# Kernel optimization log

Measured on AMD Instinct MI355X. Metric: run time of the kernel, lower is better.

Reference implementation:

```python
import jax, jax.numpy as jnp
import numpy as np

N_NODES = 100000


def _gcn_conv(x, src, dst, deg_inv_sqrt, W, b, num_nodes):
    # GCNConv: out = D^{-1/2} (A+I) D^{-1/2} (x W) + b, with self-loops already
    # appended to (src, dst) and deg_inv_sqrt precomputed over the augmented graph.
    h = x @ W                                            # [N, out]
    coef = deg_inv_sqrt[src] * deg_inv_sqrt[dst]         # [E+N]
    msg = h[src] * coef[:, None]                         # gather + normalize
    out = jax.ops.segment_sum(msg, dst, num_segments=num_nodes)  # scatter-add
    return out + b


def setup_inputs() -> dict:
    key = jax.random.key(0)
    ks = jax.random.split(key, 8)
    n, d, h = N_NODES, 16, 16
    E = 3_200_000
    x = jax.random.normal(ks[0], (n, d), dtype=jnp.float32)
    edge_index = jax.random.randint(ks[1], (2, E), 0, n, dtype=jnp.int64)
    # Glorot-ish init for weights, zeros for biases (as in GCNConv/Linear defaults)
    W1 = jax.random.normal(ks[2], (d, h), dtype=jnp.float32) / np.sqrt(d)
    b1 = jnp.zeros((h,), dtype=jnp.float32)
    W2 = jax.random.normal(ks[3], (h, h), dtype=jnp.float32) / np.sqrt(h)
    b2 = jnp.zeros((h,), dtype=jnp.float32)
    Wfc = jax.random.normal(ks[4], (h, 1), dtype=jnp.float32) / np.sqrt(h)
    bfc = jnp.zeros((1,), dtype=jnp.float32)
    return {"x": x, "edge_index": edge_index, "W1": W1, "b1": b1,
            "W2": W2, "b2": b2, "Wfc": Wfc, "bfc": bfc}


def reference(x, edge_index, W1, b1, W2, b2, Wfc, bfc):
    n = x.shape[0]
    loops = jnp.arange(n, dtype=edge_index.dtype)
    src = jnp.concatenate([edge_index[0], loops])
    dst = jnp.concatenate([edge_index[1], loops])
    # symmetric normalization over graph with self-loops (edge weight 1)
    deg = jax.ops.segment_sum(jnp.ones_like(dst, dtype=x.dtype), dst, num_segments=n)
    deg_inv_sqrt = jnp.where(deg > 0, jax.lax.rsqrt(deg), 0.0)
    h = jax.nn.relu(_gcn_conv(x, src, dst, deg_inv_sqrt, W1, b1, n))
    h = jax.nn.relu(_gcn_conv(h, src, dst, deg_inv_sqrt, W2, b2, n))
    return h @ Wfc + bfc  # [N, 1]
```

## Files before the change

### kernel.cpp

```cpp
#include <hip/hip_runtime.h>
#include <hip/hip_fp16.h>
#include <stdint.h>


constexpr int F = 16;
constexpr int K_MAX = 256;
constexpr int BN = 400;
constexpr int PT = 4096;
constexpr int NPB = 32;
constexpr unsigned int CAP = 14848;

__device__ __forceinline__ float2 h2f2(__half2 h) { return __half22float2(h); }
__device__ __forceinline__ unsigned int bkt400(unsigned int d) {
    return (unsigned int)(((unsigned long long)d * 167773ull) >> 26);
}

__global__ void __launch_bounds__(256)
partition_kernel(const int* __restrict__ src, const int* __restrict__ dst,
                 unsigned int* __restrict__ gcur, unsigned int* __restrict__ recs,
                 int E, int K) {
    __shared__ unsigned int hist[K_MAX * 4];
    __shared__ unsigned int offs[K_MAX * 4];
    __shared__ unsigned int gb[K_MAX];
    __shared__ unsigned int wsum[4];
    __shared__ unsigned int drec[PT];
    __shared__ unsigned char dbuk[PT];
    const int t = threadIdx.x;
    const int tile0 = blockIdx.x * PT;
    const int cnt = min(PT, E - tile0);
    const unsigned int myc = (unsigned int)(t & 3);
    for (int i = t; i < K * 4; i += 256) hist[i] = 0u;
    __syncthreads();
    unsigned int rec[16], bp[16];
#pragma unroll
    for (int k = 0; k < 4; ++k) {
        const int i = t * 4 + k * 1024;
        const int e = tile0 + i;
        if (i + 3 < cnt) {
            int4 s4 = *(const int4*)&src[e];
            int4 d4 = *(const int4*)&dst[e];
            int ss[4] = {s4.x, s4.y, s4.z, s4.w};
            int dd[4] = {d4.x, d4.y, d4.z, d4.w};
#pragma unroll
            for (int u = 0; u < 4; ++u) {
                unsigned int d = (unsigned int)dd[u];
                unsigned int s = (unsigned int)ss[u];
                unsigned int b = bkt400(d);
                rec[k * 4 + u] = ((d - b * (unsigned int)BN) << 17) | s;
                unsigned int pos = atomicAdd(&hist[b * 4 + myc], 1u);
                bp[k * 4 + u] = (b << 14) | (myc << 12) | pos;
            }
        } else {
#pragma unroll
            for (int u = 0; u < 4; ++u) {
                const int ii = i + u;
                bp[k * 4 + u] = 0xFFFFFFFFu;
                if (ii < cnt) {
                    unsigned int d = (unsigned int)dst[tile0 + ii];
                    unsigned int s = (unsigned int)src[tile0 + ii];
                    unsigned int b = bkt400(d);
                    rec[k * 4 + u] = ((d - b * (unsigned int)BN) << 17) | s;
                    unsigned int pos = atomicAdd(&hist[b * 4 + myc], 1u);
                    bp[k * 4 + u] = (b << 14) | (myc << 12) | pos;
                }
            }
        }
    }
    __syncthreads();
    const int lane = t & 63, wid = t >> 6;
    unsigned int tot = 0u;
    if (t < K) {
        unsigned int h0 = hist[t * 4 + 0], h1 = hist[t * 4 + 1];
        unsigned int h2 = hist[t * 4 + 2], h3 = hist[t * 4 + 3];
        tot = h0 + h1 + h2 + h3;
        offs[t * 4 + 0] = 0u;
        offs[t * 4 + 1] = h0;
        offs[t * 4 + 2] = h0 + h1;
        offs[t * 4 + 3] = h0 + h1 + h2;
    }
    unsigned int incl = tot;
#pragma unroll
    for (int o = 1; o < 64; o <<= 1) {
        unsigned int y = __shfl_up(incl, o, 64);
        if (lane >= o) incl += y;
    }
    if (lane == 63) wsum[wid] = incl;
    __syncthreads();
    if (t == 0) {
        unsigned int run = 0;
#pragma unroll
        for (int i = 0; i < 4; ++i) { unsigned int tmp = wsum[i]; wsum[i] = run; run += tmp; }
    }
    __syncthreads();
    if (t < K) {
        unsigned int bb = wsum[wid] + incl - tot;
        unsigned int g = (unsigned int)t * CAP + atomicAdd(&gcur[t], tot);
        gb[t] = g - bb;
        offs[t * 4 + 0] += bb;
        offs[t * 4 + 1] += bb;
        offs[t * 4 + 2] += bb;
        offs[t * 4 + 3] += bb;
    }
    __syncthreads();
#pragma unroll
    for (int k = 0; k < 16; ++k) {
        if (bp[k] != 0xFFFFFFFFu) {
            unsigned int b = bp[k] >> 14, c = (bp[k] >> 12) & 3u, pos = bp[k] & 0xFFFu;
            unsigned int idx = offs[b * 4 + c] + pos;
            drec[idx] = rec[k];
            dbuk[idx] = (unsigned char)b;
        }
    }
    __syncthreads();
    for (int i = t; i < cnt; i += 256) {
        unsigned int b = dbuk[i];
        recs[gb[b] + (unsigned int)i] = drec[i];
    }
}

__global__ void __launch_bounds__(1024)
sort_mv_kernel(const unsigned int* __restrict__ recs, const unsigned int* __restrict__ gcur,
               const float* __restrict__ x, const float* __restrict__ W1,
               float* __restrict__ dis, unsigned int* __restrict__ rp,
               unsigned int* __restrict__ recs2, __half* __restrict__ hs1, int N) {
    __shared__ unsigned int cnt0[BN];
    __shared__ unsigned int cnt1[BN];
    __shared__ unsigned int wsum[7];
    __shared__ float sdis[BN];
    __shared__ float ws[16][16];
    __shared__ float xs[64][17];
    __shared__ unsigned int srt[CAP];
    const int b = blockIdx.x;
    const int t = threadIdx.x;
    const int lane = t & 63, wid = t >> 6;
    if (t < BN) { cnt0[t] = 0u; cnt1[t] = 0u; }
    if (t < 256) ws[t >> 4][t & 15] = W1[t];
    __syncthreads();
    const unsigned int e0 = (unsigned int)b * CAP;
    const unsigned int len = gcur[b];
    const unsigned int len4 = len & ~3u;
    unsigned int* mycnt = (t & 1) ? cnt1 : cnt0;
    for (unsigned int i = 4u * t; i < len4; i += 4096u) {
        uint4 r4 = *(const uint4*)&recs[e0 + i];
        atomicAdd(&mycnt[r4.x >> 17], 1u);
        atomicAdd(&mycnt[r4.y >> 17], 1u);
        atomicAdd(&mycnt[r4.z >> 17], 1u);
        atomicAdd(&mycnt[r4.w >> 17], 1u);
    }
    for (unsigned int i = len4 + t; i < len; i += 1024u)
        atomicAdd(&mycnt[recs[e0 + i] >> 17], 1u);
    __syncthreads();
    unsigned int c = 0, c0v = 0, xsc = 0;
    if (t < BN) {
        c0v = cnt0[t];
        c = c0v + cnt1[t];
        xsc = c;
#pragma unroll
        for (int o = 1; o < 64; o <<= 1) {
            unsigned int y = __shfl_up(xsc, o, 64);
            if (lane >= o) xsc += y;
        }
        if (lane == 63 || t == BN - 1) wsum[wid] = xsc;
    }
    __syncthreads();
    if (t == 0) {
        unsigned int run = 0;
#pragma unroll
        for (int i = 0; i < 7; ++i) { unsigned int tmp = wsum[i]; wsum[i] = run; run += tmp; }
    }
    __syncthreads();
    if (t < BN) {
        const unsigned int srel = wsum[wid] + xsc - c;
        const int v = b * BN + t;
        const float dv = rsqrtf(1.0f + (float)c);
        sdis[t] = dv;
        if (v < N) {
            dis[v] = dv;
            rp[v] = (c << 24) | (e0 + srel);
        }
        cnt0[t] = srel;
        cnt1[t] = srel + c0v;
    }
    __syncthreads();
    for (unsigned int i = 4u * t; i < len4; i += 4096u) {
        uint4 r4 = *(const uint4*)&recs[e0 + i];
        unsigned int s0 = atomicAdd(&mycnt[r4.x >> 17], 1u);
        srt[s0] = r4.x & 0x1FFFFu;
        unsigned int s1 = atomicAdd(&mycnt[r4.y >> 17], 1u);
        srt[s1] = r4.y & 0x1FFFFu;
        unsigned int s2 = atomicAdd(&mycnt[r4.z >> 17], 1u);
        srt[s2] = r4.z & 0x1FFFFu;
        unsigned int s3 = atomicAdd(&mycnt[r4.w >> 17], 1u);
        srt[s3] = r4.w & 0x1FFFFu;
    }
    for (unsigned int i = len4 + t; i < len; i += 1024u) {
        unsigned int r = recs[e0 + i];
        unsigned int slot = atomicAdd(&mycnt[r >> 17], 1u);
        srt[slot] = r & 0x1FFFFu;
    }
    __syncthreads();
    for (unsigned int i = 4u * t; i < len4; i += 4096u) {
        uint4 vv = *(const uint4*)&srt[i];
        *(uint4*)&recs2[e0 + i] = vv;
    }
    for (unsigned int i = len4 + t; i < len; i += 1024u)
        recs2[e0 + i] = srt[i];
    const int n = t >> 4, j = t & 15;
#pragma unroll
    for (int tile = 0; tile < 7; ++tile) {
        const int loc = tile * 64 + n;
        const int node = b * BN + loc;
        __syncthreads();
        xs[n][j] = (loc < BN && node < N) ? x[(size_t)node * F + j] : 0.0f;
        __syncthreads();
        if (loc < BN && node < N) {
            float acc = 0.f;
#pragma unroll
            for (int k = 0; k < 16; ++k) acc += xs[n][k] * ws[k][j];
            hs1[(size_t)node * F + j] = __float2half(acc * sdis[loc]);
        }
    }
}

__global__ void __launch_bounds__(256)
agg1_kernel(const unsigned int* __restrict__ recs2, const unsigned int* __restrict__ rp,
            const __half2* __restrict__ hs1, const float* __restrict__ dis,
            const float* __restrict__ W2, const float* __restrict__ b1,
            __half* __restrict__ hs2, int N) {
    __shared__ float ws[16][16];
    __shared__ float hbf[NPB][17];
    const int t = threadIdx.x;
    ws[t >> 4][t & 15] = W2[t];
    const int j2 = t & 7;
    const int g8 = t >> 3;
    const int v0 = blockIdx.x * NPB;
    {
        const int v = v0 + g8;
        float sx = 0.f, sy = 0.f, dv = 0.f;
        if (v < N) {
            dv = dis[v];
            const unsigned int w = rp[v];
            unsigned int e = w & 0xFFFFFFu;
            const unsigned int e1 = e + (w >> 24);
            float2 s = h2f2(hs1[(size_t)v * 8 + j2]);
            sx = s.x; sy = s.y;
            for (; e + 8 <= e1; e += 8) {
                unsigned int r0 = recs2[e + 0], r1 = recs2[e + 1];
                unsigned int r2 = recs2[e + 2], r3 = recs2[e + 3];
                unsigned int r4 = recs2[e + 4], r5 = recs2[e + 5];
                unsigned int r6 = recs2[e + 6], r7 = recs2[e + 7];
                float2 a0 = h2f2(hs1[r0 * 8 + j2]), a1 = h2f2(hs1[r1 * 8 + j2]);
                float2 a2 = h2f2(hs1[r2 * 8 + j2]), a3 = h2f2(hs1[r3 * 8 + j2]);
                float2 a4 = h2f2(hs1[r4 * 8 + j2]), a5 = h2f2(hs1[r5 * 8 + j2]);
                float2 a6 = h2f2(hs1[r6 * 8 + j2]), a7 = h2f2(hs1[r7 * 8 + j2]);
                sx += ((a0.x + a1.x) + (a2.x + a3.x)) + ((a4.x + a5.x) + (a6.x + a7.x));
                sy += ((a0.y + a1.y) + (a2.y + a3.y)) + ((a4.y + a5.y) + (a6.y + a7.y));
            }
            for (; e < e1; ++e) {
                float2 a = h2f2(hs1[recs2[e] * 8 + j2]);
                sx += a.x; sy += a.y;
            }
        }
        hbf[g8][2 * j2 + 0] = fmaxf(dv * sx + b1[2 * j2 + 0], 0.f);
        hbf[g8][2 * j2 + 1] = fmaxf(dv * sy + b1[2 * j2 + 1], 0.f);
    }
    __syncthreads();
    const int j = t & 15;
    const int g = t >> 4;
#pragma unroll
    for (int it = 0; it < 2; ++it) {
        const int n = g + 16 * it;
        const int v = v0 + n;
        if (v >= N) continue;
        float acc = 0.f;
#pragma unroll
        for (int k = 0; k < 16; ++k) acc += hbf[n][k] * ws[k][j];
        hs2[(size_t)v * F + j] = __float2half(acc * dis[v]);
    }
}

__global__ void __launch_bounds__(256)
agg2_kernel(const unsigned int* __restrict__ recs2, const unsigned int* __restrict__ rp,
            const __half2* __restrict__ hs2, const float* __restrict__ dis,
            const float* __restrict__ b2, const float* __restrict__ Wfc,
            const float* __restrict__ bfc, float* __restrict__ out, int N) {
    const int t = threadIdx.x;
    const int j2 = t & 7;
    const int g8 = t >> 3;
    const int v0 = blockIdx.x * NPB;
    const float wfx = Wfc[2 * j2 + 0], wfy = Wfc[2 * j2 + 1];
    const float bbx = b2[2 * j2 + 0], bby = b2[2 * j2 + 1];
    const float bf = bfc[0];
    const int v = v0 + g8;
    if (v >= N) return;
    const unsigned int w = rp[v];
    unsigned int e = w & 0xFFFFFFu;
    const unsigned int e1 = e + (w >> 24);
    float2 s0 = h2f2(hs2[(size_t)v * 8 + j2]);
    float sx = s0.x, sy = s0.y;
    for (; e + 8 <= e1; e += 8) {
        unsigned int r0 = recs2[e + 0], r1 = recs2[e + 1];
        unsigned int r2 = recs2[e + 2], r3 = recs2[e + 3];
        unsigned int r4 = recs2[e + 4], r5 = recs2[e + 5];
        unsigned int r6 = recs2[e + 6], r7 = recs2[e + 7];
        float2 a0 = h2f2(hs2[r0 * 8 + j2]), a1 = h2f2(hs2[r1 * 8 + j2]);
        float2 a2 = h2f2(hs2[r2 * 8 + j2]), a3 = h2f2(hs2[r3 * 8 + j2]);
        float2 a4 = h2f2(hs2[r4 * 8 + j2]), a5 = h2f2(hs2[r5 * 8 + j2]);
        float2 a6 = h2f2(hs2[r6 * 8 + j2]), a7 = h2f2(hs2[r7 * 8 + j2]);
        sx += ((a0.x + a1.x) + (a2.x + a3.x)) + ((a4.x + a5.x) + (a6.x + a7.x));
        sy += ((a0.y + a1.y) + (a2.y + a3.y)) + ((a4.y + a5.y) + (a6.y + a7.y));
    }
    for (; e < e1; ++e) {
        float2 a = h2f2(hs2[recs2[e] * 8 + j2]);
        sx += a.x; sy += a.y;
    }
    const float dv = dis[v];
    float h = fmaxf(dv * sx + bbx, 0.f) * wfx + fmaxf(dv * sy + bby, 0.f) * wfy;
    h += __shfl_down(h, 4, 8);
    h += __shfl_down(h, 2, 8);
    h += __shfl_down(h, 1, 8);
    if (j2 == 0) out[v] = h + bf;
}

static inline char* align256(char* p) {
    return (char*)(((uintptr_t)p + 255) & ~(uintptr_t)255);
}

extern "C" void kernel_launch(void* const* d_in, const int* in_sizes, int n_in,
                              void* d_out, int out_size, void* d_ws, size_t ws_size,
                              hipStream_t stream) {
    const float* x   = (const float*)d_in[0];
    const int*   ei  = (const int*)d_in[1];
    const float* W1  = (const float*)d_in[2];
    const float* b1  = (const float*)d_in[3];
    const float* W2  = (const float*)d_in[4];
    const float* b2  = (const float*)d_in[5];
    const float* Wfc = (const float*)d_in[6];
    const float* bfc = (const float*)d_in[7];
    float* out = (float*)d_out;

    const int N = in_sizes[0] / F;
    const int E = in_sizes[1] / 2;
    const int* src = ei;
    const int* dst = ei + E;
    const int K = (N + BN - 1) / BN;

    char* p = (char*)d_ws;
    float* dis = (float*)align256(p);                   p = (char*)(dis + N);
    unsigned int* gcur  = (unsigned int*)align256(p);   p = (char*)(gcur + K);
    unsigned int* rp    = (unsigned int*)align256(p);   p = (char*)(rp + N);
    unsigned int* recs2 = (unsigned int*)align256(p);   p = (char*)(recs2 + (size_t)K * CAP);
    unsigned int* recs  = (unsigned int*)align256(p);   p = (char*)(recs + (size_t)K * CAP);
    __half* hs1 = (__half*)align256(p);                 p = (char*)(hs1 + (size_t)N * F);
    __half* hs2 = (__half*)align256(p);

    const int T = 256;

    hipMemsetAsync(gcur, 0, (size_t)K * sizeof(unsigned int), stream);
    partition_kernel<<<(E + PT - 1) / PT, T, 0, stream>>>(src, dst, gcur, recs, E, K);
    sort_mv_kernel<<<K, 1024, 0, stream>>>(recs, gcur, x, W1, dis, rp, recs2, hs1, N);
    agg1_kernel<<<(N + NPB - 1) / NPB, T, 0, stream>>>(recs2, rp, (const __half2*)hs1, dis, W2, b1, hs2, N);
    agg2_kernel<<<(N + NPB - 1) / NPB, T, 0, stream>>>(recs2, rp, (const __half2*)hs2, dis, b2, Wfc, bfc, out, N);
}
```

Before: 173.9 us.

## Compute node degrees in partition kernel via global atomics instead of recounting

The per-node degree histogram moves out of sort_mv_kernel's first pass over the bucket records and into partition_kernel. Each edge now does a global atomicAdd into a split (two-lane) degree array, and sort_mv reads those counts directly. This removes one full read of the records and a shared-memory atomic pass from the sort kernel. In exchange it adds 3.2M global atomics with scattered addresses plus a larger memset. The scatter phase now alternates counters by element position instead of by thread parity, and that position parity must line up with the gi&1 split used for the degree counts.

```diff
diff --git a/kernel.cpp b/kernel.cpp
--- a/kernel.cpp
+++ b/kernel.cpp
@@ -18,7 +18,7 @@
 __global__ void __launch_bounds__(256)
 partition_kernel(const int* __restrict__ src, const int* __restrict__ dst,
                  unsigned int* __restrict__ gcur, unsigned int* __restrict__ recs,
-                 int E, int K) {
+                 unsigned int* __restrict__ deg, int E, int K) {
     __shared__ unsigned int hist[K_MAX * 4];
     __shared__ unsigned int offs[K_MAX * 4];
     __shared__ unsigned int gb[K_MAX];
@@ -113,13 +113,18 @@
     }
     __syncthreads();
     for (int i = t; i < cnt; i += 256) {
+        unsigned int r = drec[i];
         unsigned int b = dbuk[i];
-        recs[gb[b] + (unsigned int)i] = drec[i];
+        unsigned int gi = gb[b] + (unsigned int)i;
+        recs[gi] = r;
+        unsigned int v = b * (unsigned int)BN + (r >> 17);
+        atomicAdd(&deg[v * 2u + (gi & 1u)], 1u);
     }
 }
 
 __global__ void __launch_bounds__(1024)
 sort_mv_kernel(const unsigned int* __restrict__ recs, const unsigned int* __restrict__ gcur,
+               const unsigned int* __restrict__ deg,
                const float* __restrict__ x, const float* __restrict__ W1,
                float* __restrict__ dis, unsigned int* __restrict__ rp,
                unsigned int* __restrict__ recs2, __half* __restrict__ hs1, int N) {
@@ -133,27 +138,15 @@
     const int b = blockIdx.x;
     const int t = threadIdx.x;
     const int lane = t & 63, wid = t >> 6;
-    if (t < BN) { cnt0[t] = 0u; cnt1[t] = 0u; }
     if (t < 256) ws[t >> 4][t & 15] = W1[t];
-    __syncthreads();
     const unsigned int e0 = (unsigned int)b * CAP;
     const unsigned int len = gcur[b];
     const unsigned int len4 = len & ~3u;
-    unsigned int* mycnt = (t & 1) ? cnt1 : cnt0;
-    for (unsigned int i = 4u * t; i < len4; i += 4096u) {
-        uint4 r4 = *(const uint4*)&recs[e0 + i];
-        atomicAdd(&mycnt[r4.x >> 17], 1u);
-        atomicAdd(&mycnt[r4.y >> 17], 1u);
-        atomicAdd(&mycnt[r4.z >> 17], 1u);
-        atomicAdd(&mycnt[r4.w >> 17], 1u);
-    }
-    for (unsigned int i = len4 + t; i < len; i += 1024u)
-        atomicAdd(&mycnt[recs[e0 + i] >> 17], 1u);
-    __syncthreads();
     unsigned int c = 0, c0v = 0, xsc = 0;
     if (t < BN) {
-        c0v = cnt0[t];
-        c = c0v + cnt1[t];
+        uint2 dd = *(const uint2*)&deg[2u * (unsigned int)(b * BN + t)];
+        c0v = dd.x;
+        c = dd.x + dd.y;
         xsc = c;
 #pragma unroll
         for (int o = 1; o < 64; o <<= 1) {
@@ -184,19 +177,22 @@
     __syncthreads();
     for (unsigned int i = 4u * t; i < len4; i += 4096u) {
         uint4 r4 = *(const uint4*)&recs[e0 + i];
-        unsigned int s0 = atomicAdd(&mycnt[r4.x >> 17], 1u);
+        unsigned int s0 = atomicAdd(&cnt0[r4.x >> 17], 1u);
         srt[s0] = r4.x & 0x1FFFFu;
-        unsigned int s1 = atomicAdd(&mycnt[r4.y >> 17], 1u);
+        unsigned int s1 = atomicAdd(&cnt1[r4.y >> 17], 1u);
         srt[s1] = r4.y & 0x1FFFFu;
-        unsigned int s2 = atomicAdd(&mycnt[r4.z >> 17], 1u);
+        unsigned int s2 = atomicAdd(&cnt0[r4.z >> 17], 1u);
         srt[s2] = r4.z & 0x1FFFFu;
-        unsigned int s3 = atomicAdd(&mycnt[r4.w >> 17], 1u);
+        unsigned int s3 = atomicAdd(&cnt1[r4.w >> 17], 1u);
         srt[s3] = r4.w & 0x1FFFFu;
     }
-    for (unsigned int i = len4 + t; i < len; i += 1024u) {
-        unsigned int r = recs[e0 + i];
-        unsigned int slot = atomicAdd(&mycnt[r >> 17], 1u);
-        srt[slot] = r & 0x1FFFFu;
+    {
+        unsigned int* mycnt = (t & 1) ? cnt1 : cnt0;
+        for (unsigned int i = len4 + t; i < len; i += 1024u) {
+            unsigned int r = recs[e0 + i];
+            unsigned int slot = atomicAdd(&mycnt[r >> 17], 1u);
+            srt[slot] = r & 0x1FFFFu;
+        }
     }
     __syncthreads();
     for (unsigned int i = 4u * t; i < len4; i += 4096u) {
@@ -347,7 +343,9 @@
 
     char* p = (char*)d_ws;
     float* dis = (float*)align256(p);                   p = (char*)(dis + N);
-    unsigned int* gcur  = (unsigned int*)align256(p);   p = (char*)(gcur + K);
+    unsigned int* gcur  = (unsigned int*)align256(p);
+    unsigned int* deg   = gcur + 256;
+    p = (char*)(deg + 2 * (size_t)N);
     unsigned int* rp    = (unsigned int*)align256(p);   p = (char*)(rp + N);
     unsigned int* recs2 = (unsigned int*)align256(p);   p = (char*)(recs2 + (size_t)K * CAP);
     unsigned int* recs  = (unsigned int*)align256(p);   p = (char*)(recs + (size_t)K * CAP);
@@ -356,9 +354,9 @@
 
     const int T = 256;
 
-    hipMemsetAsync(gcur, 0, (size_t)K * sizeof(unsigned int), stream);
-    partition_kernel<<<(E + PT - 1) / PT, T, 0, stream>>>(src, dst, gcur, recs, E, K);
-    sort_mv_kernel<<<K, 1024, 0, stream>>>(recs, gcur, x, W1, dis, rp, recs2, hs1, N);
+    hipMemsetAsync(gcur, 0, (256 + 2 * (size_t)N) * sizeof(unsigned int), stream);
+    partition_kernel<<<(E + PT - 1) / PT, T, 0, stream>>>(src, dst, gcur, recs, deg, E, K);
+    sort_mv_kernel<<<K, 1024, 0, stream>>>(recs, gcur, deg, x, W1, dis, rp, recs2, hs1, N);
     agg1_kernel<<<(N + NPB - 1) / NPB, T, 0, stream>>>(recs2, rp, (const __half2*)hs1, dis, W2, b1, hs2, N);
     agg2_kernel<<<(N + NPB - 1) / NPB, T, 0, stream>>>(recs2, rp, (const __half2*)hs2, dis, b2, Wfc, bfc, out, N);
 }
```

After: 277.2 us. 1.59x slower.
